# Performance work log

Hardware: AMD Instinct MI355X
Metric: run time of the kernel (lower is better)

## Reference

```python
import jax, jax.numpy as jnp
import numpy as np

DIM = 1024
NUM_HEADS = 16
SCALE = DIM ** (-0.5)  # NOTE: source scales by full dim, not head_dim


def setup_inputs() -> dict:
    key = jax.random.key(0)
    ks = jax.random.split(key, 10)
    B, N, C = 2, 2048, DIM
    s = 0.02
    return {
        "x": jax.random.normal(ks[0], (B, N, C), dtype=jnp.float32),
        "queries": jax.random.normal(ks[1], (B, N, C), dtype=jnp.float32),
        "wq": jax.random.normal(ks[2], (C, C), dtype=jnp.float32) * s,
        "bq": jnp.zeros((C,), dtype=jnp.float32),
        "wk": jax.random.normal(ks[3], (C, C), dtype=jnp.float32) * s,
        "bk": jnp.zeros((C,), dtype=jnp.float32),
        "wv": jax.random.normal(ks[4], (C, C), dtype=jnp.float32) * s,
        "bv": jnp.zeros((C,), dtype=jnp.float32),
        "wo": jax.random.normal(ks[5], (C, C), dtype=jnp.float32) * s,
        "bo": jnp.zeros((C,), dtype=jnp.float32),
    }


def reference(x, queries, wq, bq, wk, bk, wv, bv, wo, bo):
    B, N, C = queries.shape
    H = NUM_HEADS
    D = C // H
    # torch Linear: y = x @ W.T + b  (W is [out, in])
    q = (queries @ wq.T + bq).reshape(B, N, H, D).transpose(0, 2, 1, 3)  # [B,H,N,D]
    k = (x @ wk.T + bk).reshape(B, N, H, D).transpose(0, 2, 1, 3)
    v = (x @ wv.T + bv).reshape(B, N, H, D).transpose(0, 2, 1, 3)
    attn = jnp.einsum("bhqd,bhkd->bhqk", q, k) * SCALE  # full-dim scale per source
    attn = jax.nn.softmax(attn, axis=-1)
    out = jnp.einsum("bhqk,bhkd->bhqd", attn, v)  # [B,H,N,D]
    out = out.transpose(0, 2, 1, 3).reshape(B, N, C)
    return out @ wo.T + bo
```

## Files before the change

### kernel.cpp

```cpp
#include <hip/hip_runtime.h>
#include <hip/hip_bf16.h>

typedef __attribute__((ext_vector_type(8))) short bf16x8;
typedef __attribute__((ext_vector_type(4))) float f32x4;
typedef unsigned short u16;
typedef unsigned int u32;

#define MFMA16(a,b,c) __builtin_amdgcn_mfma_f32_16x16x32_bf16((a),(b),(c),0,0,0)

#if defined(__has_builtin) && __has_builtin(__builtin_amdgcn_exp2f)
#define EXP2(x) __builtin_amdgcn_exp2f(x)
#else
#define EXP2(x) exp2f(x)
#endif

#define QSCALE 0.045084220027780106f

__device__ __forceinline__ u16 f2bf(float f) {
  union { float f; unsigned int u; } v; v.f = f;
  unsigned int r = v.u + 0x7FFFu + ((v.u >> 16) & 1u);
  return (u16)(r >> 16);
}

__device__ __forceinline__ u32 pkbf(float a, float b) {
  union { __hip_bfloat162 h; u32 u; } cv;
  cv.h = __float22bfloat162_rn(make_float2(a, b));
  return cv.u;
}

__device__ __forceinline__ void gld16(const void* g, void* l) {
  __builtin_amdgcn_global_load_lds(
      (__attribute__((address_space(1))) void*)(g),
      (__attribute__((address_space(3))) void*)(l), 16, 0, 0);
}

__global__ __launch_bounds__(256) void cast_all(
    const float* __restrict__ x, const float* __restrict__ qu,
    const float* __restrict__ wq, const float* __restrict__ wk,
    const float* __restrict__ wv, const float* __restrict__ wo,
    u16* __restrict__ xb, u16* __restrict__ qub,
    u16* __restrict__ wqb, u16* __restrict__ wkb,
    u16* __restrict__ wvb, u16* __restrict__ wob)
{
  int i = blockIdx.x * 256 + threadIdx.x;
  const float4* src; u16* dst; int off;
  if (i < 1048576)      { src = (const float4*)qu; dst = qub; off = i; }
  else if (i < 2097152) { src = (const float4*)x;  dst = xb;  off = i - 1048576; }
  else if (i < 2359296) { src = (const float4*)wq; dst = wqb; off = i - 2097152; }
  else if (i < 2621440) { src = (const float4*)wk; dst = wkb; off = i - 2359296; }
  else if (i < 2883584) { src = (const float4*)wv; dst = wvb; off = i - 2621440; }
  else                  { src = (const float4*)wo; dst = wob; off = i - 2883584; }
  float4 v = src[off];
  ushort4 r; r.x = f2bf(v.x); r.y = f2bf(v.y); r.z = f2bf(v.z); r.w = f2bf(v.w);
  ((ushort4*)dst)[off] = r;
}

__global__ __launch_bounds__(256) void gemm_qkv(
    const u16* __restrict__ qub, const u16* __restrict__ xb,
    const u16* __restrict__ wqb, const u16* __restrict__ wkb, const u16* __restrict__ wvb,
    const float* __restrict__ bq, const float* __restrict__ bk, const float* __restrict__ bv,
    u16* __restrict__ qhd, u16* __restrict__ khd, u16* __restrict__ vtd)
{
  __shared__ u16 As[128 * 64];
  __shared__ u16 Bs[128 * 64];
  int tid = threadIdx.x, w = tid >> 6, lane = tid & 63;
  int c = lane & 15, quad = lane >> 4;
  int bm = blockIdx.x, bn = blockIdx.y, z = blockIdx.z;
  int wm = w >> 1, wn = w & 1;
  const u16* A = (z == 0) ? qub : xb;
  const u16* W = (z == 0) ? wqb : (z == 1) ? wkb : wvb;
  f32x4 acc[4][4] = {};
  for (int k0 = 0; k0 < 1024; k0 += 64) {
#pragma unroll
    for (int i = 0; i < 4; i++) {
      int seg = i * 256 + w * 64 + lane;
      int row = seg >> 3, pseg = seg & 7;
      int lseg = pseg ^ (row & 7);
      gld16(A + (size_t)(bm * 128 + row) * 1024 + k0 + lseg * 8,
            &As[(i * 256 + w * 64) * 8]);
      gld16(W + (size_t)(bn * 128 + row) * 1024 + k0 + lseg * 8,
            &Bs[(i * 256 + w * 64) * 8]);
    }
    __syncthreads();
#pragma unroll
    for (int ks = 0; ks < 2; ks++) {
      bf16x8 af[4], bfr[4];
#pragma unroll
      for (int mt = 0; mt < 4; mt++) {
        int row = wm * 64 + mt * 16 + c;
        int cseg = (ks * 4 + quad) ^ (row & 7);
        af[mt] = *(const bf16x8*)&As[(row * 8 + cseg) * 8];
      }
#pragma unroll
      for (int nt = 0; nt < 4; nt++) {
        int row = wn * 64 + nt * 16 + c;
        int cseg = (ks * 4 + quad) ^ (row & 7);
        bfr[nt] = *(const bf16x8*)&Bs[(row * 8 + cseg) * 8];
      }
      if (z < 2) {
#pragma unroll
        for (int ct = 0; ct < 4; ct++)
#pragma unroll
          for (int tt = 0; tt < 4; tt++)
            acc[ct][tt] = MFMA16(bfr[ct], af[tt], acc[ct][tt]);
      } else {
#pragma unroll
        for (int mt = 0; mt < 4; mt++)
#pragma unroll
          for (int nt = 0; nt < 4; nt++)
            acc[mt][nt] = MFMA16(af[mt], bfr[nt], acc[mt][nt]);
      }
    }
    __syncthreads();
  }
  if (z < 2) {
    const float* bias = (z == 0) ? bq : bk;
    u16* dst = (z == 0) ? qhd : khd;
    float sc = (z == 0) ? QSCALE : 1.0f;
    float4 bbs[4];
#pragma unroll
    for (int ct = 0; ct < 4; ct++) {
      float4 b4 = *(const float4*)&bias[bn * 128 + wn * 64 + ct * 16 + quad * 4];
      bbs[ct].x = b4.x * sc; bbs[ct].y = b4.y * sc;
      bbs[ct].z = b4.z * sc; bbs[ct].w = b4.w * sc;
    }
#pragma unroll
    for (int ct = 0; ct < 4; ct++) {
      int ch = bn * 128 + wn * 64 + ct * 16 + quad * 4;
      int h = ch >> 6, d0 = ch & 63;
#pragma unroll
      for (int tt = 0; tt < 4; tt++) {
        int tok = bm * 128 + wm * 64 + tt * 16 + c;
        int b = tok >> 11, n = tok & 2047;
        float v0 = fmaf(acc[ct][tt][0], sc, bbs[ct].x);
        float v1 = fmaf(acc[ct][tt][1], sc, bbs[ct].y);
        float v2 = fmaf(acc[ct][tt][2], sc, bbs[ct].z);
        float v3 = fmaf(acc[ct][tt][3], sc, bbs[ct].w);
        uint2 pk; pk.x = pkbf(v0, v1); pk.y = pkbf(v2, v3);
        *(uint2*)&dst[((size_t)(b * 16 + h) * 2048 + n) * 64 + d0] = pk;
      }
    }
  } else {
    float bval[4];
#pragma unroll
    for (int nt = 0; nt < 4; nt++)
      bval[nt] = bv[bn * 128 + wn * 64 + nt * 16 + c];
#pragma unroll
    for (int mt = 0; mt < 4; mt++) {
      int tokl = (mt & 2) * 16 + quad * 8 + (mt & 1) * 4;
      int tok = bm * 128 + wm * 64 + tokl;
      int b = tok >> 11, np = tok & 2047;
#pragma unroll
      for (int nt = 0; nt < 4; nt++) {
        int ch = bn * 128 + wn * 64 + nt * 16 + c;
        int h = ch >> 6, d = ch & 63;
        float v0 = acc[mt][nt][0] + bval[nt];
        float v1 = acc[mt][nt][1] + bval[nt];
        float v2 = acc[mt][nt][2] + bval[nt];
        float v3 = acc[mt][nt][3] + bval[nt];
        uint2 pk; pk.x = pkbf(v0, v1); pk.y = pkbf(v2, v3);
        *(uint2*)&vtd[((size_t)(b * 16 + h) * 64 + d) * 2048 + np] = pk;
      }
    }
  }
}

__global__ __launch_bounds__(128) void attn(
    const u16* __restrict__ qh, const u16* __restrict__ kh,
    const u16* __restrict__ vt, u16* __restrict__ ot)
{
  __shared__ u16 Kbuf[2][64 * 64];
  __shared__ u16 Vbuf[2][64 * 64];
  int tid = threadIdx.x, w = tid >> 6, lane = tid & 63;
  int c = lane & 15, quad = lane >> 4;
  int bh = blockIdx.x, qt = blockIdx.y;
  const u16* qp = qh + ((size_t)bh * 2048 + qt * 64 + w * 32) * 64;

  bf16x8 Qf[2][2];
#pragma unroll
  for (int qt2 = 0; qt2 < 2; qt2++)
#pragma unroll
    for (int ks = 0; ks < 2; ks++)
      Qf[qt2][ks] = *(const bf16x8*)(qp + (size_t)(qt2 * 16 + c) * 64 + ks * 32 + quad * 8);

  int off0 = c * 64 + ((quad) ^ (c & 7)) * 8;
  int off1 = c * 64 + ((4 + quad) ^ (c & 7)) * 8;

  int sr = lane >> 3;
  int row0 = w * 8 + sr;
  int sls = (lane & 7) ^ (sr & 7);
  const u16* kg = kh + (size_t)bh * 2048 * 64 + row0 * 64 + sls * 8;
  const u16* vg = vt + (size_t)bh * 64 * 2048 + row0 * 2048 + sls * 8;

#define STAGE(B)                                                                \
  {                                                                             \
    gld16(kg,          &Kbuf[B][(w * 64) * 8]);                                 \
    gld16(kg + 1024,   &Kbuf[B][(128 + w * 64) * 8]);                           \
    gld16(kg + 2048,   &Kbuf[B][(256 + w * 64) * 8]);                           \
    gld16(kg + 3072,   &Kbuf[B][(384 + w * 64) * 8]);                           \
    gld16(vg,          &Vbuf[B][(w * 64) * 8]);                                 \
    gld16(vg + 32768,  &Vbuf[B][(128 + w * 64) * 8]);                           \
    gld16(vg + 65536,  &Vbuf[B][(256 + w * 64) * 8]);                           \
    gld16(vg + 98304,  &Vbuf[B][(384 + w * 64) * 8]);                           \
    kg += 4096; vg += 64;                                                       \
  }

  STAGE(0)
  __syncthreads();

  f32x4 O[2][4] = {};
  f32x4 Lacc[2] = {};
  bf16x8 vone;
#pragma unroll
  for (int j = 0; j < 8; j++) vone[j] = (short)0x3F80;

#define ITER(PH, PREF)                                                          \
  {                                                                             \
    if (PREF) STAGE(PH ^ 1)                                                     \
    const u16* Ks = Kbuf[PH];                                                   \
    const u16* Vs = Vbuf[PH];                                                   \
    bf16x8 Kf[4][2];                                                            \
    _Pragma("unroll") for (int nt = 0; nt < 4; nt++) {                          \
      Kf[nt][0] = *(const bf16x8*)&Ks[off0 + nt * 1024];                        \
      Kf[nt][1] = *(const bf16x8*)&Ks[off1 + nt * 1024];                        \
    }                                                                           \
    f32x4 S[2][4] = {};                                                         \
    _Pragma("unroll") for (int qt2 = 0; qt2 < 2; qt2++)                         \
      _Pragma("unroll") for (int nt = 0; nt < 4; nt++) {                        \
        S[qt2][nt] = MFMA16(Kf[nt][0], Qf[qt2][0], S[qt2][nt]);                 \
        S[qt2][nt] = MFMA16(Kf[nt][1], Qf[qt2][1], S[qt2][nt]);                 \
      }                                                                         \
    bf16x8 pa[2][2];                                                            \
    _Pragma("unroll") for (int qt2 = 0; qt2 < 2; qt2++)                         \
      _Pragma("unroll") for (int i = 0; i < 2; i++) {                           \
        float e0 = EXP2(S[qt2][2 * i][0]), e1 = EXP2(S[qt2][2 * i][1]);         \
        float e2 = EXP2(S[qt2][2 * i][2]), e3 = EXP2(S[qt2][2 * i][3]);         \
        float e4 = EXP2(S[qt2][2 * i + 1][0]), e5 = EXP2(S[qt2][2 * i + 1][1]); \
        float e6 = EXP2(S[qt2][2 * i + 1][2]), e7 = EXP2(S[qt2][2 * i + 1][3]); \
        union { uint4 u; bf16x8 v; } cv;                                        \
        cv.u.x = pkbf(e0, e1); cv.u.y = pkbf(e2, e3);                           \
        cv.u.z = pkbf(e4, e5); cv.u.w = pkbf(e6, e7);                           \
        pa[qt2][i] = cv.v;                                                      \
      }                                                                         \
    Lacc[0] = MFMA16(pa[0][0], vone, Lacc[0]);                                  \
    Lacc[0] = MFMA16(pa[0][1], vone, Lacc[0]);                                  \
    Lacc[1] = MFMA16(pa[1][0], vone, Lacc[1]);                                  \
    Lacc[1] = MFMA16(pa[1][1], vone, Lacc[1]);                                  \
    bf16x8 Vf[4][2];                                                            \
    _Pragma("unroll") for (int dt = 0; dt < 4; dt++) {                          \
      Vf[dt][0] = *(const bf16x8*)&Vs[off0 + dt * 1024];                        \
      Vf[dt][1] = *(const bf16x8*)&Vs[off1 + dt * 1024];                        \
    }                                                                           \
    _Pragma("unroll") for (int qt2 = 0; qt2 < 2; qt2++)                         \
      _Pragma("unroll") for (int dt = 0; dt < 4; dt++) {                        \
        O[qt2][dt] = MFMA16(pa[qt2][0], Vf[dt][0], O[qt2][dt]);                 \
        O[qt2][dt] = MFMA16(pa[qt2][1], Vf[dt][1], O[qt2][dt]);                 \
      }                                                                         \
    __syncthreads();                                                            \
  }

  for (int kt2 = 0; kt2 < 15; kt2++) {
    ITER(0, 1)
    ITER(1, 1)
  }
  ITER(0, 1)
  ITER(1, 0)
#undef ITER
#undef STAGE

  int b_ = bh >> 4, h = bh & 15;
#pragma unroll
  for (int qt2 = 0; qt2 < 2; qt2++) {
    f32x4 linv;
#pragma unroll
    for (int j = 0; j < 4; j++) linv[j] = 1.0f / Lacc[qt2][j];
#pragma unroll
    for (int j = 0; j < 4; j++) {
      int n = qt * 64 + w * 32 + qt2 * 16 + quad * 4 + j;
      u16* op = ot + (((size_t)b_ * 2048 + n) * 16 + h) * 64;
#pragma unroll
      for (int dt = 0; dt < 4; dt++)
        op[dt * 16 + c] = f2bf(O[qt2][dt][j] * linv[j]);
    }
  }
}

__global__ __launch_bounds__(256) void gemm_out(
    const u16* __restrict__ Aot, const u16* __restrict__ wob,
    const float* __restrict__ bo, float* __restrict__ out)
{
  __shared__ u16 As[64 * 64];
  __shared__ u16 Bs[128 * 64];
  int tid = threadIdx.x, w = tid >> 6, lane = tid & 63;
  int bm = blockIdx.x, bn = blockIdx.y;
  int wm = w >> 1, wn = w & 1;
  f32x4 acc[2][4] = {};
  for (int k0 = 0; k0 < 1024; k0 += 64) {
#pragma unroll
    for (int i = 0; i < 2; i++) {
      int seg = i * 256 + tid;
      int row = seg >> 3, pseg = seg & 7;
      int lseg = pseg ^ (row & 7);
      gld16(Aot + (size_t)(bm * 64 + row) * 1024 + k0 + lseg * 8,
            &As[(i * 256 + tid - (tid & 7)) * 8 + (tid & 7) * 8]);
    }
#pragma unroll
    for (int i = 0; i < 4; i++) {
      int seg = i * 256 + tid;
      int row = seg >> 3, pseg = seg & 7;
      int lseg = pseg ^ (row & 7);
      gld16(wob + (size_t)(bn * 128 + row) * 1024 + k0 + lseg * 8,
            &Bs[(i * 256 + tid - (tid & 7)) * 8 + (tid & 7) * 8]);
    }
    __syncthreads();
#pragma unroll
    for (int ks = 0; ks < 2; ks++) {
      bf16x8 af[2], bfr[4];
#pragma unroll
      for (int mt = 0; mt < 2; mt++) {
        int row = wm * 32 + mt * 16 + (lane & 15);
        int cseg = (ks * 4 + (lane >> 4)) ^ (row & 7);
        af[mt] = *(const bf16x8*)&As[(row * 8 + cseg) * 8];
      }
#pragma unroll
      for (int nt = 0; nt < 4; nt++) {
        int row = wn * 64 + nt * 16 + (lane & 15);
        int cseg = (ks * 4 + (lane >> 4)) ^ (row & 7);
        bfr[nt] = *(const bf16x8*)&Bs[(row * 8 + cseg) * 8];
      }
#pragma unroll
      for (int mt = 0; mt < 2; mt++)
#pragma unroll
        for (int nt = 0; nt < 4; nt++)
          acc[mt][nt] = MFMA16(af[mt], bfr[nt], acc[mt][nt]);
    }
    __syncthreads();
  }
#pragma unroll
  for (int nt = 0; nt < 4; nt++) {
    int o = bn * 128 + wn * 64 + nt * 16 + (lane & 15);
    float bval = bo[o];
#pragma unroll
    for (int mt = 0; mt < 2; mt++)
#pragma unroll
      for (int j = 0; j < 4; j++) {
        int m = bm * 64 + wm * 32 + mt * 16 + (lane >> 4) * 4 + j;
        out[(size_t)m * 1024 + o] = acc[mt][nt][j] + bval;
      }
  }
}

extern "C" void kernel_launch(void* const* d_in, const int* in_sizes, int n_in,
                              void* d_out, int out_size, void* d_ws, size_t ws_size,
                              hipStream_t stream)
{
  const float* x  = (const float*)d_in[0];
  const float* qu = (const float*)d_in[1];
  const float* wq = (const float*)d_in[2];
  const float* bq = (const float*)d_in[3];
  const float* wk = (const float*)d_in[4];
  const float* bk = (const float*)d_in[5];
  const float* wv = (const float*)d_in[6];
  const float* bv = (const float*)d_in[7];
  const float* wo = (const float*)d_in[8];
  const float* bo = (const float*)d_in[9];
  float* out = (float*)d_out;
  char* ws = (char*)d_ws;
  u16* xb  = (u16*)(ws + (size_t)0);
  u16* qub = (u16*)(ws + ((size_t)8  << 20));
  u16* wqb = (u16*)(ws + ((size_t)16 << 20));
  u16* wkb = (u16*)(ws + ((size_t)18 << 20));
  u16* wvb = (u16*)(ws + ((size_t)20 << 20));
  u16* wob = (u16*)(ws + ((size_t)22 << 20));
  u16* qhd = (u16*)(ws + ((size_t)24 << 20));
  u16* khd = (u16*)(ws + ((size_t)32 << 20));
  u16* vtd = (u16*)(ws + ((size_t)40 << 20));
  u16* otd = (u16*)(ws + ((size_t)48 << 20));

  cast_all<<<12288, 256, 0, stream>>>(x, qu, wq, wk, wv, wo,
                                      xb, qub, wqb, wkb, wvb, wob);
  gemm_qkv<<<dim3(32, 8, 3), 256, 0, stream>>>(qub, xb, wqb, wkb, wvb,
                                               bq, bk, bv, qhd, khd, vtd);
  attn<<<dim3(32, 32), 128, 0, stream>>>(qhd, khd, vtd, otd);
  gemm_out<<<dim3(64, 8), 256, 0, stream>>>(otd, wob, bo, out);
}
```

Measured before the change: 204.6 us.

## Restructure attention K/V prefetch pipeline with explicit vmcnt waits and MFMA priority

Replaces the __syncthreads-based double-buffered loop with explicit s_barrier plus sched_barrier fences and a partial s_waitcnt vmcnt(8). This lets the next tile's global-to-LDS loads stay in flight while the current tile computes, instead of draining all outstanding loads at each block barrier. It also raises wave priority around the MFMA blocks and moves the row-sum MFMAs next to the PV MFMAs. The hand-written waitcnt counts rely on the exact number of async loads per stage, which is fragile, and the extra barriers add per-iteration sync cost.

```diff
diff --git a/kernel.cpp b/kernel.cpp
--- a/kernel.cpp
+++ b/kernel.cpp
@@ -205,8 +205,13 @@
     kg += 4096; vg += 64;                                                       \
   }
 
-  STAGE(0)
-  __syncthreads();
+#define SB __builtin_amdgcn_sched_barrier(0);
+#define BARR  SB __builtin_amdgcn_s_barrier(); SB
+#define PIPE(B)                                                                 \
+  BARR                                                                          \
+  STAGE(B)                                                                      \
+  SB asm volatile("s_waitcnt vmcnt(8)" ::: "memory"); SB                        \
+  BARR
 
   f32x4 O[2][4] = {};
   f32x4 Lacc[2] = {};
@@ -214,9 +219,8 @@
 #pragma unroll
   for (int j = 0; j < 8; j++) vone[j] = (short)0x3F80;
 
-#define ITER(PH, PREF)                                                          \
+#define COMPUTE(PH)                                                             \
   {                                                                             \
-    if (PREF) STAGE(PH ^ 1)                                                     \
     const u16* Ks = Kbuf[PH];                                                   \
     const u16* Vs = Vbuf[PH];                                                   \
     bf16x8 Kf[4][2];                                                            \
@@ -225,11 +229,13 @@
       Kf[nt][1] = *(const bf16x8*)&Ks[off1 + nt * 1024];                        \
     }                                                                           \
     f32x4 S[2][4] = {};                                                         \
+    __builtin_amdgcn_s_setprio(1);                                              \
     _Pragma("unroll") for (int qt2 = 0; qt2 < 2; qt2++)                         \
       _Pragma("unroll") for (int nt = 0; nt < 4; nt++) {                        \
         S[qt2][nt] = MFMA16(Kf[nt][0], Qf[qt2][0], S[qt2][nt]);                 \
         S[qt2][nt] = MFMA16(Kf[nt][1], Qf[qt2][1], S[qt2][nt]);                 \
       }                                                                         \
+    __builtin_amdgcn_s_setprio(0);                                              \
     bf16x8 pa[2][2];                                                            \
     _Pragma("unroll") for (int qt2 = 0; qt2 < 2; qt2++)                         \
       _Pragma("unroll") for (int i = 0; i < 2; i++) {                           \
@@ -242,30 +248,38 @@
         cv.u.z = pkbf(e4, e5); cv.u.w = pkbf(e6, e7);                           \
         pa[qt2][i] = cv.v;                                                      \
       }                                                                         \
-    Lacc[0] = MFMA16(pa[0][0], vone, Lacc[0]);                                  \
-    Lacc[0] = MFMA16(pa[0][1], vone, Lacc[0]);                                  \
-    Lacc[1] = MFMA16(pa[1][0], vone, Lacc[1]);                                  \
-    Lacc[1] = MFMA16(pa[1][1], vone, Lacc[1]);                                  \
     bf16x8 Vf[4][2];                                                            \
     _Pragma("unroll") for (int dt = 0; dt < 4; dt++) {                          \
       Vf[dt][0] = *(const bf16x8*)&Vs[off0 + dt * 1024];                        \
       Vf[dt][1] = *(const bf16x8*)&Vs[off1 + dt * 1024];                        \
     }                                                                           \
+    __builtin_amdgcn_s_setprio(1);                                              \
+    Lacc[0] = MFMA16(pa[0][0], vone, Lacc[0]);                                  \
+    Lacc[0] = MFMA16(pa[0][1], vone, Lacc[0]);                                  \
+    Lacc[1] = MFMA16(pa[1][0], vone, Lacc[1]);                                  \
+    Lacc[1] = MFMA16(pa[1][1], vone, Lacc[1]);                                  \
     _Pragma("unroll") for (int qt2 = 0; qt2 < 2; qt2++)                         \
       _Pragma("unroll") for (int dt = 0; dt < 4; dt++) {                        \
         O[qt2][dt] = MFMA16(pa[qt2][0], Vf[dt][0], O[qt2][dt]);                 \
         O[qt2][dt] = MFMA16(pa[qt2][1], Vf[dt][1], O[qt2][dt]);                 \
       }                                                                         \
-    __syncthreads();                                                            \
-  }
-
+    __builtin_amdgcn_s_setprio(0);                                              \
+  }
+
+  STAGE(0)
   for (int kt2 = 0; kt2 < 15; kt2++) {
-    ITER(0, 1)
-    ITER(1, 1)
-  }
-  ITER(0, 1)
-  ITER(1, 0)
-#undef ITER
+    PIPE(1) COMPUTE(0)
+    PIPE(0) COMPUTE(1)
+  }
+  PIPE(1) COMPUTE(0)
+  BARR
+  SB asm volatile("s_waitcnt vmcnt(0)" ::: "memory"); SB
+  BARR
+  COMPUTE(1)
+#undef COMPUTE
+#undef PIPE
+#undef BARR
+#undef SB
 #undef STAGE
 
   int b_ = bh >> 4, h = bh & 15;
```

Measured after the change: 208.2 us. About the same (+1.7%).
